# Optimization experiments

Hardware: AMD Instinct MI355X
Metric: run time of the kernel (lower is better)

## Reference

```python
import jax, jax.numpy as jnp
import numpy as np

N = 262144          # flattened node batch
IN_S, IN_V = 256, 32
OUT_S, OUT_V = 256, 32
H = max(IN_V, OUT_V)  # 32
EPS = 1e-4


def setup_inputs() -> dict:
    key = jax.random.key(0)
    ks = jax.random.split(key, 8)
    inv = lambda f: 1.0 / np.sqrt(f).astype(np.float32)
    return {
        "s": jax.random.normal(ks[0], (N, IN_S), jnp.float32),
        "V": jax.random.normal(ks[1], (N, IN_V, 3), jnp.float32),
        "W_h": jax.random.normal(ks[2], (H, IN_V), jnp.float32) * inv(IN_V),
        "W_mu": jax.random.normal(ks[3], (OUT_V, H), jnp.float32) * inv(H),
        "W_m_w": jax.random.normal(ks[4], (OUT_S, H + IN_S), jnp.float32) * inv(H + IN_S),
        "W_m_b": jax.random.normal(ks[5], (OUT_S,), jnp.float32) * 0.01,
        "W_g_w": jax.random.normal(ks[6], (OUT_V, OUT_S), jnp.float32) * inv(OUT_S),
        "W_g_b": jax.random.normal(ks[7], (OUT_V,), jnp.float32) * 0.01,
    }


def reference(s, V, W_h, W_mu, W_m_w, W_m_b, W_g_w, W_g_b):
    # V_h = W_h @ V : [N, H, 3]
    V_h = jnp.einsum('hv,nvc->nhc', W_h, V)
    # per-row L2 norm, clipped at eps : [N, H]
    s_h = jnp.maximum(jnp.linalg.norm(V_h, axis=-1), EPS)
    # Linear on concatenated scalars : [N, OUT_S]
    s_m = jnp.concatenate([s, s_h], axis=-1) @ W_m_w.T + W_m_b
    s_dash = jax.nn.relu(s_m)                      # sigma = relu
    # V_mu = W_mu @ V_h : [N, OUT_V, 3]
    V_mu = jnp.einsum('mh,nhc->nmc', W_mu, V_h)
    # vector gate: sigmoid(W_g(sigmoid(s_m)))  (sigma_plus = sigmoid)
    gate = jax.nn.sigmoid(jax.nn.sigmoid(s_m) @ W_g_w.T + W_g_b)  # [N, OUT_V]
    V_dash = gate[..., None] * V_mu
    return s_dash, V_dash
```

## Files before the change

kernel.cpp:

```cpp
#include <hip/hip_runtime.h>

#define NTOT 262144
#define BN   32
#define NT   256
#define SXS  296
#define VTS  36

typedef __attribute__((ext_vector_type(8))) short bf16x8;
typedef __attribute__((ext_vector_type(4))) float f32x4;

static __device__ __forceinline__ unsigned short f2b(float x) {
    union { float f; unsigned u; } c; c.f = x;
    unsigned r = c.u + 0x7FFFu + ((c.u >> 16) & 1u);
    return (unsigned short)(r >> 16);
}
static __device__ __forceinline__ bf16x8 cvt8(const float* p) {
    float4 x = *(const float4*)p, y = *(const float4*)(p + 4);
    bf16x8 r;
    r[0] = (short)f2b(x.x); r[1] = (short)f2b(x.y); r[2] = (short)f2b(x.z); r[3] = (short)f2b(x.w);
    r[4] = (short)f2b(y.x); r[5] = (short)f2b(y.y); r[6] = (short)f2b(y.z); r[7] = (short)f2b(y.w);
    return r;
}
static __device__ __forceinline__ void glds16(const unsigned short* g, void* l) {
    __builtin_amdgcn_global_load_lds(
        (const __attribute__((address_space(1))) void*)g,
        (__attribute__((address_space(3))) void*)l, 16, 0, 0);
}

__global__ void pack_w(const float* __restrict__ Wmw, const float* __restrict__ Wgw,
                       unsigned short* __restrict__ wp) {
    int t = blockIdx.x * 256 + threadIdx.x;
    if (t < 73728) {
        int o = t / 288, k = t % 288;
        int ks = k >> 5, kk = k & 31, q = o >> 6, ol = o & 63;
        int kks = kk ^ (((ol >> 1) & 3) << 3);
        wp[(ks * 4 + q) * 2048 + ol * 32 + kks] = f2b(Wmw[t]);
    } else if (t < 81920) {
        int j = t - 73728;
        int o = j >> 8, k = j & 255;
        wp[73728 + (k >> 5) * 1024 + o * 32 + (k & 31)] = f2b(Wgw[j]);
    }
}

template<int USE_WS>
__global__ __launch_bounds__(NT, 3)
void gvp_main(const float* __restrict__ s, const float* __restrict__ V,
              const float* __restrict__ Wh, const float* __restrict__ Wmu,
              const float* __restrict__ Wmw, const float* __restrict__ Wmb,
              const float* __restrict__ Wgw, const float* __restrict__ Wgb,
              const unsigned short* __restrict__ wpack,
              float* __restrict__ out)
{
    __shared__ __attribute__((aligned(16))) unsigned short sX[BN * SXS];
    __shared__ __attribute__((aligned(16))) unsigned short sWb[3 * 2048];
    __shared__ __attribute__((aligned(16))) unsigned short sVT[96 * VTS];

    const int t  = threadIdx.x;
    const int w  = t >> 6, l = t & 63;
    const int fr = l & 15, fq = l >> 4;
    const int n0 = blockIdx.x * BN;
    const int half = w & 1, oh = w >> 1;

    if (USE_WS) {
        #pragma unroll
        for (int c = 0; c < 3; ++c)
            glds16(wpack + c * 2048 + w * 512 + l * 8, &sWb[c * 2048 + w * 512]);
    }

    #pragma unroll
    for (int i = 0; i < 8; ++i) {
        int n = i * 4 + w;
        float4 x4 = *(const float4*)&s[(size_t)(n0 + n) * 256 + 4 * l];
        ushort4 h4; h4.x = f2b(x4.x); h4.y = f2b(x4.y); h4.z = f2b(x4.z); h4.w = f2b(x4.w);
        *(ushort4*)&sX[n * SXS + 4 * l] = h4;
    }
    {
        int n = t >> 3, vq = t & 7;
        const float* p = &V[(size_t)(n0 + n) * 96 + vq * 12];
        float4 q0 = *(const float4*)(p);
        float4 q1 = *(const float4*)(p + 4);
        float4 q2 = *(const float4*)(p + 8);
        ushort4 c0 = { f2b(q0.x), f2b(q0.w), f2b(q1.z), f2b(q2.y) };
        ushort4 c1 = { f2b(q0.y), f2b(q1.x), f2b(q1.w), f2b(q2.z) };
        ushort4 c2 = { f2b(q0.z), f2b(q1.y), f2b(q2.x), f2b(q2.w) };
        *(ushort4*)&sVT[(0 * 32 + n) * VTS + vq * 4] = c0;
        *(ushort4*)&sVT[(1 * 32 + n) * VTS + vq * 4] = c1;
        *(ushort4*)&sVT[(2 * 32 + n) * VTS + vq * 4] = c2;
    }
    if (!USE_WS) {
        #pragma unroll
        for (int c = 0; c < 3; ++c) {
            int ol = w * 16 + (l >> 2), kh = l & 3, x = (ol >> 1) & 3;
            const float* p = &Wmw[(c * 64 + ol) * 288 + kh * 8];
            sWb[c * 2048 + 0] = sWb[c * 2048 + 0];
            *(bf16x8*)&sWb[c * 2048 + ol * 32 + ((kh ^ x) << 3)] = cvt8(p);
        }
    }
    __syncthreads();

    {
        bf16x8 bh = cvt8(&Wh[(oh * 16 + fr) * 32 + fq * 8]);
        f32x4 va0 = {0,0,0,0}, va1 = {0,0,0,0}, va2 = {0,0,0,0};
        bf16x8 a0 = *(const bf16x8*)&sVT[(0 * 32 + half * 16 + fr) * VTS + fq * 8];
        bf16x8 a1 = *(const bf16x8*)&sVT[(1 * 32 + half * 16 + fr) * VTS + fq * 8];
        bf16x8 a2 = *(const bf16x8*)&sVT[(2 * 32 + half * 16 + fr) * VTS + fq * 8];
        va0 = __builtin_amdgcn_mfma_f32_16x16x32_bf16(a0, bh, va0, 0, 0, 0);
        va1 = __builtin_amdgcn_mfma_f32_16x16x32_bf16(a1, bh, va1, 0, 0, 0);
        va2 = __builtin_amdgcn_mfma_f32_16x16x32_bf16(a2, bh, va2, 0, 0, 0);
        __syncthreads();
        #pragma unroll
        for (int r = 0; r < 4; ++r) {
            int nl = half * 16 + fq * 4 + r;
            int h  = oh * 16 + fr;
            sVT[(0 * 32 + nl) * VTS + h] = f2b(va0[r]);
            sVT[(1 * 32 + nl) * VTS + h] = f2b(va1[r]);
            sVT[(2 * 32 + nl) * VTS + h] = f2b(va2[r]);
            float nrm = sqrtf(fmaf(va0[r], va0[r], fmaf(va1[r], va1[r], va2[r] * va2[r])));
            sX[nl * SXS + 256 + h] = f2b(fmaxf(nrm, 1e-4f));
        }
    }
    __syncthreads();

    f32x4 acc[2][4];
    #pragma unroll
    for (int mt = 0; mt < 2; ++mt)
        #pragma unroll
        for (int j = 0; j < 4; ++j) acc[mt][j] = (f32x4){0.f, 0.f, 0.f, 0.f};

    const int ol0 = w * 16 + fr;
    const int bo0 = ol0 * 32 + ((fq ^ ((ol0 >> 1) & 3)) << 3);

    #pragma unroll
    for (int ks = 0; ks < 9; ++ks) {
        bf16x8 a0 = *(const bf16x8*)&sX[fr * SXS + ks * 32 + fq * 8];
        bf16x8 a1 = *(const bf16x8*)&sX[(16 + fr) * SXS + ks * 32 + fq * 8];
        #pragma unroll
        for (int q = 0; q < 4; ++q) {
            const int qi = ks * 4 + q;
            if (qi >= 3) {
                if (qi <= 33)      asm volatile("s_waitcnt vmcnt(2)" ::: "memory");
                else if (qi == 34) asm volatile("s_waitcnt vmcnt(1)" ::: "memory");
                else               asm volatile("s_waitcnt vmcnt(0)" ::: "memory");
                __builtin_amdgcn_sched_barrier(0);
            }
            const unsigned short* bw = &sWb[(qi % 3) * 2048];
            bf16x8 b0 = *(const bf16x8*)&bw[bo0];
            if (qi <= 32) {
                asm volatile("s_waitcnt lgkmcnt(0)" ::: "memory");
                __builtin_amdgcn_sched_barrier(0);
                if (USE_WS) {
                    glds16(wpack + (qi + 3) * 2048 + w * 512 + l * 8,
                           &sWb[(qi % 3) * 2048 + w * 512]);
                } else {
                    int qc = qi + 3, ks2 = qc >> 2, q2 = qc & 3;
                    int ol = w * 16 + (l >> 2), kh = l & 3, x = (ol >> 1) & 3;
                    const float* p = &Wmw[(q2 * 64 + ol) * 288 + ks2 * 32 + kh * 8];
                    *(bf16x8*)&sWb[(qi % 3) * 2048 + ol * 32 + ((kh ^ x) << 3)] = cvt8(p);
                }
            }
            acc[0][q] = __builtin_amdgcn_mfma_f32_16x16x32_bf16(a0, b0, acc[0][q], 0, 0, 0);
            acc[1][q] = __builtin_amdgcn_mfma_f32_16x16x32_bf16(a1, b0, acc[1][q], 0, 0, 0);
        }
    }
    __syncthreads();

    float bias[4];
    #pragma unroll
    for (int q = 0; q < 4; ++q) bias[q] = Wmb[q * 64 + w * 16 + fr];

    #pragma unroll
    for (int mt = 0; mt < 2; ++mt)
        #pragma unroll
        for (int q = 0; q < 4; ++q) {
            int col = q * 64 + w * 16 + fr;
            #pragma unroll
            for (int r = 0; r < 4; ++r) {
                int node = mt * 16 + fq * 4 + r;
                float m = acc[mt][q][r] + bias[q];
                sX[node * SXS + col] = f2b(1.f / (1.f + __expf(-m)));
            }
        }
    __syncthreads();

    float gate[4];
    {
        f32x4 g = (f32x4){0.f, 0.f, 0.f, 0.f};
        #pragma unroll
        for (int ks = 0; ks < 8; ++ks) {
            bf16x8 a = *(const bf16x8*)&sX[(half * 16 + fr) * SXS + ks * 32 + fq * 8];
            bf16x8 b;
            if (USE_WS) b = *(const bf16x8*)&wpack[73728 + ks * 1024 + (oh * 16 + fr) * 32 + fq * 8];
            else        b = cvt8(&Wgw[(oh * 16 + fr) * 256 + ks * 32 + fq * 8]);
            g = __builtin_amdgcn_mfma_f32_16x16x32_bf16(a, b, g, 0, 0, 0);
        }
        float gb = Wgb[oh * 16 + fr];
        #pragma unroll
        for (int r = 0; r < 4; ++r)
            gate[r] = 1.f / (1.f + __expf(-(g[r] + gb)));
    }
    __syncthreads();

    const int skw = ((fq & 1) << 4) | ((fq >> 1) << 3);
    float* sRel = (float*)sX;
    #pragma unroll
    for (int mt = 0; mt < 2; ++mt) {
        #pragma unroll
        for (int r = 0; r < 4; ++r) {
            int row = fq * 4 + r;
            #pragma unroll
            for (int q = 0; q < 4; ++q) {
                int col = q * 64 + w * 16 + fr;
                sRel[row * 256 + (col ^ skw)] = fmaxf(acc[mt][q][r] + bias[q], 0.f);
            }
        }
        __syncthreads();
        #pragma unroll
        for (int i = 0; i < 4; ++i) {
            int flat = i * NT + t;
            int row = flat >> 6, c4 = flat & 63;
            int sk2 = (((row >> 2) & 1) << 4) | (((row >> 3) & 1) << 3);
            float4 v4 = *(const float4*)&sRel[row * 256 + ((c4 * 4) ^ sk2)];
            *(float4*)&out[(size_t)(n0 + mt * 16 + row) * 256 + c4 * 4] = v4;
        }
        __syncthreads();
    }

    float* sc = (float*)sX;
    {
        bf16x8 bm = cvt8(&Wmu[(oh * 16 + fr) * 32 + fq * 8]);
        f32x4 m0 = {0,0,0,0}, m1 = {0,0,0,0}, m2 = {0,0,0,0};
        bf16x8 a0 = *(const bf16x8*)&sVT[(0 * 32 + half * 16 + fr) * VTS + fq * 8];
        bf16x8 a1 = *(const bf16x8*)&sVT[(1 * 32 + half * 16 + fr) * VTS + fq * 8];
        bf16x8 a2 = *(const bf16x8*)&sVT[(2 * 32 + half * 16 + fr) * VTS + fq * 8];
        m0 = __builtin_amdgcn_mfma_f32_16x16x32_bf16(a0, bm, m0, 0, 0, 0);
        m1 = __builtin_amdgcn_mfma_f32_16x16x32_bf16(a1, bm, m1, 0, 0, 0);
        m2 = __builtin_amdgcn_mfma_f32_16x16x32_bf16(a2, bm, m2, 0, 0, 0);
        #pragma unroll
        for (int r = 0; r < 4; ++r) {
            int node = half * 16 + fq * 4 + r;
            int m    = oh * 16 + fr;
            sc[node * 96 + m * 3 + 0] = gate[r] * m0[r];
            sc[node * 96 + m * 3 + 1] = gate[r] * m1[r];
            sc[node * 96 + m * 3 + 2] = gate[r] * m2[r];
        }
    }
    __syncthreads();
    const size_t VBASE = (size_t)NTOT * 256;
    #pragma unroll
    for (int i = 0; i < 3; ++i) {
        int f = i * NT + t;
        *(float4*)&out[VBASE + (size_t)n0 * 96 + f * 4] = *(const float4*)&sc[f * 4];
    }
}

extern "C" void kernel_launch(void* const* d_in, const int* in_sizes, int n_in,
                              void* d_out, int out_size, void* d_ws, size_t ws_size,
                              hipStream_t stream) {
    const float* s   = (const float*)d_in[0];
    const float* V   = (const float*)d_in[1];
    const float* Wh  = (const float*)d_in[2];
    const float* Wmu = (const float*)d_in[3];
    const float* Wmw = (const float*)d_in[4];
    const float* Wmb = (const float*)d_in[5];
    const float* Wgw = (const float*)d_in[6];
    const float* Wgb = (const float*)d_in[7];
    float* out = (float*)d_out;

    dim3 grid(NTOT / BN);
    dim3 block(NT);

    if (ws_size >= 163840) {
        pack_w<<<320, 256, 0, stream>>>(Wmw, Wgw, (unsigned short*)d_ws);
        gvp_main<1><<<grid, block, 0, stream>>>(s, V, Wh, Wmu, Wmw, Wmb, Wgw, Wgb,
                                                (const unsigned short*)d_ws, out);
    } else {
        gvp_main<0><<<grid, block, 0, stream>>>(s, V, Wh, Wmu, Wmw, Wmb, Wgw, Wgb,
                                                nullptr, out);
    }
}
```

Before: 216.7 us.

## Double block to 64 nodes with two wave groups and write s_dash directly

Each block now handles 64 nodes using 512 threads split into two independent 4-wave groups, each with its own weight ring buffer and V staging. The LDS-staged, swizzled write of the relu output is replaced by direct per-element scalar global stores from the MFMA accumulators, which removes two barrier-separated passes. The cost is uncoalesced 4-byte global stores scattered across rows and lower occupancy (launch bound of 2 blocks of 512 threads).

New measurement: 219.1 us. About the same (+1.1%).

```diff
diff --git a/kernel.cpp b/kernel.cpp
--- a/kernel.cpp
+++ b/kernel.cpp
@@ -1,8 +1,8 @@
 #include <hip/hip_runtime.h>
 
 #define NTOT 262144
-#define BN   32
-#define NT   256
+#define BN   64
+#define NT   512
 #define SXS  296
 #define VTS  36
 
@@ -43,7 +43,7 @@
 }
 
 template<int USE_WS>
-__global__ __launch_bounds__(NT, 3)
+__global__ __launch_bounds__(NT, 2)
 void gvp_main(const float* __restrict__ s, const float* __restrict__ V,
               const float* __restrict__ Wh, const float* __restrict__ Wmu,
               const float* __restrict__ Wmw, const float* __restrict__ Wmb,
@@ -52,30 +52,33 @@
               float* __restrict__ out)
 {
     __shared__ __attribute__((aligned(16))) unsigned short sX[BN * SXS];
-    __shared__ __attribute__((aligned(16))) unsigned short sWb[3 * 2048];
-    __shared__ __attribute__((aligned(16))) unsigned short sVT[96 * VTS];
+    __shared__ __attribute__((aligned(16))) unsigned short sWb[2 * 3 * 2048];
+    __shared__ __attribute__((aligned(16))) unsigned short sVT[192 * VTS];
 
     const int t  = threadIdx.x;
     const int w  = t >> 6, l = t & 63;
     const int fr = l & 15, fq = l >> 4;
     const int n0 = blockIdx.x * BN;
-    const int half = w & 1, oh = w >> 1;
+    const int g  = w >> 2, wg = w & 3;
+    const int half = wg & 1, oh = wg >> 1;
 
     if (USE_WS) {
         #pragma unroll
         for (int c = 0; c < 3; ++c)
-            glds16(wpack + c * 2048 + w * 512 + l * 8, &sWb[c * 2048 + w * 512]);
+            glds16(wpack + c * 2048 + wg * 512 + l * 8,
+                   &sWb[(g * 3 + c) * 2048 + wg * 512]);
     }
 
     #pragma unroll
     for (int i = 0; i < 8; ++i) {
-        int n = i * 4 + w;
+        int n = i * 8 + w;
         float4 x4 = *(const float4*)&s[(size_t)(n0 + n) * 256 + 4 * l];
         ushort4 h4; h4.x = f2b(x4.x); h4.y = f2b(x4.y); h4.z = f2b(x4.z); h4.w = f2b(x4.w);
         *(ushort4*)&sX[n * SXS + 4 * l] = h4;
     }
     {
         int n = t >> 3, vq = t & 7;
+        int gg = n >> 5, nn = n & 31;
         const float* p = &V[(size_t)(n0 + n) * 96 + vq * 12];
         float4 q0 = *(const float4*)(p);
         float4 q1 = *(const float4*)(p + 4);
@@ -83,17 +86,16 @@
         ushort4 c0 = { f2b(q0.x), f2b(q0.w), f2b(q1.z), f2b(q2.y) };
         ushort4 c1 = { f2b(q0.y), f2b(q1.x), f2b(q1.w), f2b(q2.z) };
         ushort4 c2 = { f2b(q0.z), f2b(q1.y), f2b(q2.x), f2b(q2.w) };
-        *(ushort4*)&sVT[(0 * 32 + n) * VTS + vq * 4] = c0;
-        *(ushort4*)&sVT[(1 * 32 + n) * VTS + vq * 4] = c1;
-        *(ushort4*)&sVT[(2 * 32 + n) * VTS + vq * 4] = c2;
+        *(ushort4*)&sVT[(gg * 96 + 0 * 32 + nn) * VTS + vq * 4] = c0;
+        *(ushort4*)&sVT[(gg * 96 + 1 * 32 + nn) * VTS + vq * 4] = c1;
+        *(ushort4*)&sVT[(gg * 96 + 2 * 32 + nn) * VTS + vq * 4] = c2;
     }
     if (!USE_WS) {
         #pragma unroll
         for (int c = 0; c < 3; ++c) {
-            int ol = w * 16 + (l >> 2), kh = l & 3, x = (ol >> 1) & 3;
+            int ol = wg * 16 + (l >> 2), kh = l & 3, x = (ol >> 1) & 3;
             const float* p = &Wmw[(c * 64 + ol) * 288 + kh * 8];
-            sWb[c * 2048 + 0] = sWb[c * 2048 + 0];
-            *(bf16x8*)&sWb[c * 2048 + ol * 32 + ((kh ^ x) << 3)] = cvt8(p);
+            *(bf16x8*)&sWb[(g * 3 + c) * 2048 + ol * 32 + ((kh ^ x) << 3)] = cvt8(p);
         }
     }
     __syncthreads();
@@ -101,9 +103,9 @@
     {
         bf16x8 bh = cvt8(&Wh[(oh * 16 + fr) * 32 + fq * 8]);
         f32x4 va0 = {0,0,0,0}, va1 = {0,0,0,0}, va2 = {0,0,0,0};
-        bf16x8 a0 = *(const bf16x8*)&sVT[(0 * 32 + half * 16 + fr) * VTS + fq * 8];
-        bf16x8 a1 = *(const bf16x8*)&sVT[(1 * 32 + half * 16 + fr) * VTS + fq * 8];
-        bf16x8 a2 = *(const bf16x8*)&sVT[(2 * 32 + half * 16 + fr) * VTS + fq * 8];
+        bf16x8 a0 = *(const bf16x8*)&sVT[(g * 96 + 0 * 32 + half * 16 + fr) * VTS + fq * 8];
+        bf16x8 a1 = *(const bf16x8*)&sVT[(g * 96 + 1 * 32 + half * 16 + fr) * VTS + fq * 8];
+        bf16x8 a2 = *(const bf16x8*)&sVT[(g * 96 + 2 * 32 + half * 16 + fr) * VTS + fq * 8];
         va0 = __builtin_amdgcn_mfma_f32_16x16x32_bf16(a0, bh, va0, 0, 0, 0);
         va1 = __builtin_amdgcn_mfma_f32_16x16x32_bf16(a1, bh, va1, 0, 0, 0);
         va2 = __builtin_amdgcn_mfma_f32_16x16x32_bf16(a2, bh, va2, 0, 0, 0);
@@ -112,11 +114,11 @@
         for (int r = 0; r < 4; ++r) {
             int nl = half * 16 + fq * 4 + r;
             int h  = oh * 16 + fr;
-            sVT[(0 * 32 + nl) * VTS + h] = f2b(va0[r]);
-            sVT[(1 * 32 + nl) * VTS + h] = f2b(va1[r]);
-            sVT[(2 * 32 + nl) * VTS + h] = f2b(va2[r]);
+            sVT[(g * 96 + 0 * 32 + nl) * VTS + h] = f2b(va0[r]);
+            sVT[(g * 96 + 1 * 32 + nl) * VTS + h] = f2b(va1[r]);
+            sVT[(g * 96 + 2 * 32 + nl) * VTS + h] = f2b(va2[r]);
             float nrm = sqrtf(fmaf(va0[r], va0[r], fmaf(va1[r], va1[r], va2[r] * va2[r])));
-            sX[nl * SXS + 256 + h] = f2b(fmaxf(nrm, 1e-4f));
+            sX[(g * 32 + nl) * SXS + 256 + h] = f2b(fmaxf(nrm, 1e-4f));
         }
     }
     __syncthreads();
@@ -127,13 +129,13 @@
         #pragma unroll
         for (int j = 0; j < 4; ++j) acc[mt][j] = (f32x4){0.f, 0.f, 0.f, 0.f};
 
-    const int ol0 = w * 16 + fr;
+    const int ol0 = wg * 16 + fr;
     const int bo0 = ol0 * 32 + ((fq ^ ((ol0 >> 1) & 3)) << 3);
 
     #pragma unroll
     for (int ks = 0; ks < 9; ++ks) {
-        bf16x8 a0 = *(const bf16x8*)&sX[fr * SXS + ks * 32 + fq * 8];
-        bf16x8 a1 = *(const bf16x8*)&sX[(16 + fr) * SXS + ks * 32 + fq * 8];
+        bf16x8 a0 = *(const bf16x8*)&sX[(g * 32 + fr) * SXS + ks * 32 + fq * 8];
+        bf16x8 a1 = *(const bf16x8*)&sX[(g * 32 + 16 + fr) * SXS + ks * 32 + fq * 8];
         #pragma unroll
         for (int q = 0; q < 4; ++q) {
             const int qi = ks * 4 + q;
@@ -143,19 +145,19 @@
                 else               asm volatile("s_waitcnt vmcnt(0)" ::: "memory");
                 __builtin_amdgcn_sched_barrier(0);
             }
-            const unsigned short* bw = &sWb[(qi % 3) * 2048];
+            const unsigned short* bw = &sWb[(g * 3 + qi % 3) * 2048];
             bf16x8 b0 = *(const bf16x8*)&bw[bo0];
             if (qi <= 32) {
                 asm volatile("s_waitcnt lgkmcnt(0)" ::: "memory");
                 __builtin_amdgcn_sched_barrier(0);
                 if (USE_WS) {
-                    glds16(wpack + (qi + 3) * 2048 + w * 512 + l * 8,
-                           &sWb[(qi % 3) * 2048 + w * 512]);
+                    glds16(wpack + (qi + 3) * 2048 + wg * 512 + l * 8,
+                           &sWb[(g * 3 + qi % 3) * 2048 + wg * 512]);
                 } else {
                     int qc = qi + 3, ks2 = qc >> 2, q2 = qc & 3;
-                    int ol = w * 16 + (l >> 2), kh = l & 3, x = (ol >> 1) & 3;
+                    int ol = wg * 16 + (l >> 2), kh = l & 3, x = (ol >> 1) & 3;
                     const float* p = &Wmw[(q2 * 64 + ol) * 288 + ks2 * 32 + kh * 8];
-                    *(bf16x8*)&sWb[(qi % 3) * 2048 + ol * 32 + ((kh ^ x) << 3)] = cvt8(p);
+                    *(bf16x8*)&sWb[(g * 3 + qi % 3) * 2048 + ol * 32 + ((kh ^ x) << 3)] = cvt8(p);
                 }
             }
             acc[0][q] = __builtin_amdgcn_mfma_f32_16x16x32_bf16(a0, b0, acc[0][q], 0, 0, 0);
@@ -166,82 +168,58 @@
 
     float bias[4];
     #pragma unroll
-    for (int q = 0; q < 4; ++q) bias[q] = Wmb[q * 64 + w * 16 + fr];
+    for (int q = 0; q < 4; ++q) bias[q] = Wmb[q * 64 + wg * 16 + fr];
 
     #pragma unroll
     for (int mt = 0; mt < 2; ++mt)
         #pragma unroll
-        for (int q = 0; q < 4; ++q) {
-            int col = q * 64 + w * 16 + fr;
+        for (int r = 0; r < 4; ++r) {
+            int gn = g * 32 + mt * 16 + fq * 4 + r;
             #pragma unroll
-            for (int r = 0; r < 4; ++r) {
-                int node = mt * 16 + fq * 4 + r;
+            for (int q = 0; q < 4; ++q) {
+                int col = q * 64 + wg * 16 + fr;
                 float m = acc[mt][q][r] + bias[q];
-                sX[node * SXS + col] = f2b(1.f / (1.f + __expf(-m)));
+                sX[gn * SXS + col] = f2b(1.f / (1.f + __expf(-m)));
+                out[(size_t)(n0 + gn) * 256 + col] = fmaxf(m, 0.f);
             }
         }
     __syncthreads();
 
     float gate[4];
     {
-        f32x4 g = (f32x4){0.f, 0.f, 0.f, 0.f};
+        f32x4 ga = (f32x4){0.f, 0.f, 0.f, 0.f};
         #pragma unroll
         for (int ks = 0; ks < 8; ++ks) {
-            bf16x8 a = *(const bf16x8*)&sX[(half * 16 + fr) * SXS + ks * 32 + fq * 8];
+            bf16x8 a = *(const bf16x8*)&sX[(g * 32 + half * 16 + fr) * SXS + ks * 32 + fq * 8];
             bf16x8 b;
             if (USE_WS) b = *(const bf16x8*)&wpack[73728 + ks * 1024 + (oh * 16 + fr) * 32 + fq * 8];
             else        b = cvt8(&Wgw[(oh * 16 + fr) * 256 + ks * 32 + fq * 8]);
-            g = __builtin_amdgcn_mfma_f32_16x16x32_bf16(a, b, g, 0, 0, 0);
+            ga = __builtin_amdgcn_mfma_f32_16x16x32_bf16(a, b, ga, 0, 0, 0);
         }
         float gb = Wgb[oh * 16 + fr];
         #pragma unroll
         for (int r = 0; r < 4; ++r)
-            gate[r] = 1.f / (1.f + __expf(-(g[r] + gb)));
-    }
-    __syncthreads();
-
-    const int skw = ((fq & 1) << 4) | ((fq >> 1) << 3);
-    float* sRel = (float*)sX;
-    #pragma unroll
-    for (int mt = 0; mt < 2; ++mt) {
-        #pragma unroll
-        for (int r = 0; r < 4; ++r) {
-            int row = fq * 4 + r;
-            #pragma unroll
-            for (int q = 0; q < 4; ++q) {
-                int col = q * 64 + w * 16 + fr;
-                sRel[row * 256 + (col ^ skw)] = fmaxf(acc[mt][q][r] + bias[q], 0.f);
-            }
-        }
-        __syncthreads();
-        #pragma unroll
-        for (int i = 0; i < 4; ++i) {
-            int flat = i * NT + t;
-            int row = flat >> 6, c4 = flat & 63;
-            int sk2 = (((row >> 2) & 1) << 4) | (((row >> 3) & 1) << 3);
-            float4 v4 = *(const float4*)&sRel[row * 256 + ((c4 * 4) ^ sk2)];
-            *(float4*)&out[(size_t)(n0 + mt * 16 + row) * 256 + c4 * 4] = v4;
-        }
-        __syncthreads();
-    }
+            gate[r] = 1.f / (1.f + __expf(-(ga[r] + gb)));
+    }
+    __syncthreads();
 
     float* sc = (float*)sX;
     {
         bf16x8 bm = cvt8(&Wmu[(oh * 16 + fr) * 32 + fq * 8]);
         f32x4 m0 = {0,0,0,0}, m1 = {0,0,0,0}, m2 = {0,0,0,0};
-        bf16x8 a0 = *(const bf16x8*)&sVT[(0 * 32 + half * 16 + fr) * VTS + fq * 8];
-        bf16x8 a1 = *(const bf16x8*)&sVT[(1 * 32 + half * 16 + fr) * VTS + fq * 8];
-        bf16x8 a2 = *(const bf16x8*)&sVT[(2 * 32 + half * 16 + fr) * VTS + fq * 8];
+        bf16x8 a0 = *(const bf16x8*)&sVT[(g * 96 + 0 * 32 + half * 16 + fr) * VTS + fq * 8];
+        bf16x8 a1 = *(const bf16x8*)&sVT[(g * 96 + 1 * 32 + half * 16 + fr) * VTS + fq * 8];
+        bf16x8 a2 = *(const bf16x8*)&sVT[(g * 96 + 2 * 32 + half * 16 + fr) * VTS + fq * 8];
         m0 = __builtin_amdgcn_mfma_f32_16x16x32_bf16(a0, bm, m0, 0, 0, 0);
         m1 = __builtin_amdgcn_mfma_f32_16x16x32_bf16(a1, bm, m1, 0, 0, 0);
         m2 = __builtin_amdgcn_mfma_f32_16x16x32_bf16(a2, bm, m2, 0, 0, 0);
         #pragma unroll
         for (int r = 0; r < 4; ++r) {
-            int node = half * 16 + fq * 4 + r;
-            int m    = oh * 16 + fr;
-            sc[node * 96 + m * 3 + 0] = gate[r] * m0[r];
-            sc[node * 96 + m * 3 + 1] = gate[r] * m1[r];
-            sc[node * 96 + m * 3 + 2] = gate[r] * m2[r];
+            int gn = g * 32 + half * 16 + fq * 4 + r;
+            int m  = oh * 16 + fr;
+            sc[gn * 96 + m * 3 + 0] = gate[r] * m0[r];
+            sc[gn * 96 + m * 3 + 1] = gate[r] * m1[r];
+            sc[gn * 96 + m * 3 + 2] = gate[r] * m2[r];
         }
     }
     __syncthreads();
@@ -249,7 +227,7 @@
     #pragma unroll
     for (int i = 0; i < 3; ++i) {
         int f = i * NT + t;
-        *(float4*)&out[VBASE + (size_t)n0 * 96 + f * 4] = *(const float4*)&sc[f * 4];
+        *(float4*)&out[VBASE + (size_t)n0 * 96 + f * 4] = *(const float4*)&((float*)sX)[f * 4];
     }
 }
 
```
